# Kernel tuning notes

Hardware: AMD Instinct MI355X
Metric: run time of the kernel (lower is better)

## Reference

```python
import jax, jax.numpy as jnp
import numpy as np

B, L, DIM = 2, 1024, 512
HEADS = 8
D = DIM // HEADS
FORE_DIM, POST_DIM = 256, 1024
L_FORE, L_POST = 4 * L, L // 4


def setup_inputs() -> dict:
    key = jax.random.key(0)
    ks = jax.random.split(key, 8)
    s = 0.02  # weight init scale
    return {
        "x": jax.random.normal(ks[0], (B, L, DIM), jnp.float32),
        "fore_x": jax.random.normal(ks[1], (B, L_FORE, FORE_DIM), jnp.float32),
        "post_x": jax.random.normal(ks[2], (B, L_POST, POST_DIM), jnp.float32),
        # Linear weights stored [in, out] (transposed vs torch nn.Linear)
        "wq": jax.random.normal(ks[3], (DIM, DIM), jnp.float32) * s,
        "bq": jnp.zeros((DIM,), jnp.float32),
        "wkv1": jax.random.normal(ks[4], (FORE_DIM, 2 * DIM), jnp.float32) * s,
        "bkv1": jnp.zeros((2 * DIM,), jnp.float32),
        "wkv2": jax.random.normal(ks[5], (POST_DIM, 2 * DIM), jnp.float32) * s,
        "bkv2": jnp.zeros((2 * DIM,), jnp.float32),
        "wproj": jax.random.normal(ks[6], (3 * DIM, DIM), jnp.float32) * s,
        "bproj": jnp.zeros((DIM,), jnp.float32),
    }


def reference(x, fore_x, post_x, wq, bq, wkv1, bkv1, wkv2, bkv2, wproj, bproj):
    scale = D ** (-0.5)
    # q: [B, H, L, D], pre-scaled as in the torch code
    q = (x @ wq + bq).reshape(B, L, HEADS, D).transpose(0, 2, 1, 3) * scale

    def cross_attn(ctx, w, b):
        # ctx: [B, Lc, Cin] -> k, v: [B, H, Lc, D]
        kv = (ctx @ w + b).reshape(B, ctx.shape[1], 2, HEADS, D)
        k = kv[:, :, 0].transpose(0, 2, 1, 3)
        v = kv[:, :, 1].transpose(0, 2, 1, 3)
        attn = jax.nn.softmax(jnp.einsum("bhqd,bhkd->bhqk", q, k), axis=-1)
        out = jnp.einsum("bhqk,bhkd->bhqd", attn, v)
        return out.transpose(0, 2, 1, 3).reshape(B, L, DIM)

    x_2 = cross_attn(post_x, wkv2, bkv2)
    x_1 = cross_attn(fore_x, wkv1, bkv1)
    cat = jnp.concatenate([x, x_1, x_2], axis=2)  # [B, L, 3*DIM]
    return cat @ wproj + bproj
```

## Files before the change

kernel.cpp:

```cpp
#include <hip/hip_runtime.h>
#include <hip/hip_bf16.h>
#include <stdint.h>

typedef __attribute__((ext_vector_type(8))) short bf8;
typedef __attribute__((ext_vector_type(4))) short bf4;
typedef __attribute__((ext_vector_type(2))) short bf2;
typedef __attribute__((ext_vector_type(4))) float f32x4;

__device__ inline short f2bf(float f) {
  union { __hip_bfloat16 h; short s; } u;
  u.h = __float2bfloat16(f);
  return u.s;
}
__device__ inline float bf2f(short s) {
  union { short s; __hip_bfloat16 h; } u;
  u.s = s;
  return __bfloat162float(u.h);
}

__device__ inline f32x4 mfma16(bf8 a, bf8 b, f32x4 c) {
  return __builtin_amdgcn_mfma_f32_16x16x32_bf16(a, b, c, 0, 0, 0);
}

__global__ __launch_bounds__(256) void mega1_k(
    const float* __restrict__ x, const float* __restrict__ fore,
    const float* __restrict__ post,
    const float* __restrict__ wq, const float* __restrict__ wkv1,
    const float* __restrict__ bkv1, const float* __restrict__ wkv2,
    const float* __restrict__ wproj,
    short* __restrict__ kv1, short* __restrict__ cat,
    float* __restrict__ qpart, float* __restrict__ kv2part,
    short* __restrict__ wT)
{
  __shared__ __align__(16) short a_lds[2][128 * 40];
  __shared__ __align__(16) short b_lds[2][64 * 40];
  const int bid = blockIdx.x, tid = threadIdx.x;

  if (bid >= 1536) {
    float (*tl)[65] = reinterpret_cast<float(*)[65]>(&a_lds[0][0]);
    int tb = bid - 1536;
    int kt = tb % 24, nt = tb / 24;
    int k0 = kt * 64, n0 = nt * 64;
    int kr = tid >> 2, c4 = tid & 3;
#pragma unroll
    for (int i = 0; i < 4; ++i) {
      int cc = c4 + i * 4;
      float4 v = *(const float4*)&wproj[(size_t)(k0 + kr) * 512 + n0 + cc * 4];
      tl[kr][cc * 4 + 0] = v.x; tl[kr][cc * 4 + 1] = v.y;
      tl[kr][cc * 4 + 2] = v.z; tl[kr][cc * 4 + 3] = v.w;
    }
    __syncthreads();
    int nr = tid >> 2, p = tid & 3;
#pragma unroll
    for (int i = 0; i < 2; ++i) {
      int kk = p * 16 + i * 8;
      bf8 o;
#pragma unroll
      for (int j = 0; j < 8; ++j) o[j] = f2bf(tl[kk + j][nr]);
      *(bf8*)&wT[(size_t)(n0 + nr) * 1536 + k0 + kk] = o;
    }
    return;
  }

  const float *A, *W, *bias = nullptr;
  short* out = nullptr;
  float* outf = nullptr;
  int N, lda, ldo, m0, n0, koff;
  bool wcat = false, bf16out;
  if (bid < 1024) {
    A = fore; W = wkv1; bias = bkv1; out = kv1;
    N = 1024; lda = 256; ldo = 1024; koff = 0;
    m0 = (bid >> 4) * 128; n0 = (bid & 15) * 64; bf16out = true;
  } else if (bid < 1280) {
    int j = bid - 1024; int kc = j >> 7; j &= 127;
    A = x; W = wq; outf = qpart + (size_t)kc * (2048 * 512);
    N = 512; lda = 512; ldo = 512; koff = kc * 256;
    m0 = (j >> 3) * 128; n0 = (j & 7) * 64; bf16out = false;
    wcat = (j & 7) == 0;
  } else {
    int j = bid - 1280; int kc = j >> 6; j &= 63;
    A = post; W = wkv2; outf = kv2part + (size_t)kc * (512 * 1024);
    N = 1024; lda = 1024; ldo = 1024; koff = kc * 256;
    m0 = (j >> 4) * 128; n0 = (j & 15) * 64; bf16out = false;
  }

  const int w = tid >> 6, lane = tid & 63, g = lane >> 4, lr = lane & 15;
  const int wrow = w & 1, wcol = w >> 1;

  f32x4 z = {0.f, 0.f, 0.f, 0.f};
  f32x4 acc[4][2];
#pragma unroll
  for (int mi = 0; mi < 4; ++mi)
#pragma unroll
    for (int ni = 0; ni < 2; ++ni) acc[mi][ni] = z;

  const int arow = tid >> 3, ac4 = tid & 7;
  const int bcol = tid & 63, bj4 = tid >> 6;

  float4 ra[4], rna[4];
  float rw[8], rnw[8];

  auto LOADA = [&](int kg, float4* af, float* wg) {
#pragma unroll
    for (int i = 0; i < 4; ++i)
      af[i] = *(const float4*)&A[(size_t)(m0 + arow + 32 * i) * lda + kg + ac4 * 4];
#pragma unroll
    for (int j = 0; j < 8; ++j)
      wg[j] = W[(size_t)(kg + bj4 * 8 + j) * N + n0 + bcol];
  };
  auto STAGE = [&](int b, const float4* af, const float* wg, int kg) {
#pragma unroll
    for (int i = 0; i < 4; ++i) {
      int rr = arow + 32 * i;
      int s = (ac4 >> 1) ^ (rr & 3);
      bf4 o;
      o[0] = f2bf(af[i].x); o[1] = f2bf(af[i].y);
      o[2] = f2bf(af[i].z); o[3] = f2bf(af[i].w);
      *(bf4*)&a_lds[b][rr * 40 + s * 8 + (ac4 & 1) * 4] = o;
      if (wcat)
        *(bf4*)&cat[(size_t)(m0 + rr) * 1536 + kg + ac4 * 4] = o;
    }
    int s = bj4 ^ (bcol & 3);
    bf8 o;
#pragma unroll
    for (int j = 0; j < 8; ++j) o[j] = f2bf(wg[j]);
    *(bf8*)&b_lds[b][bcol * 40 + s * 8] = o;
  };

  LOADA(koff, ra, rw);
  STAGE(0, ra, rw, koff);
  LOADA(koff + 32, rna, rnw);
  __syncthreads();

#pragma unroll
  for (int it = 0; it < 8; ++it) {
    if (it < 7) STAGE((it + 1) & 1, rna, rnw, koff + (it + 1) * 32);
    if (it < 6) LOADA(koff + (it + 2) * 32, rna, rnw);

    const int b = it & 1;
    bf8 afr[4], bfr[2];
#pragma unroll
    for (int mi = 0; mi < 4; ++mi) {
      int row = wrow * 64 + mi * 16 + lr;
      afr[mi] = *(const bf8*)&a_lds[b][row * 40 + ((g ^ (row & 3)) << 3)];
    }
#pragma unroll
    for (int ni = 0; ni < 2; ++ni) {
      int col = wcol * 32 + ni * 16 + lr;
      bfr[ni] = *(const bf8*)&b_lds[b][col * 40 + ((g ^ (col & 3)) << 3)];
    }
#pragma unroll
    for (int mi = 0; mi < 4; ++mi)
#pragma unroll
      for (int ni = 0; ni < 2; ++ni)
        acc[mi][ni] = mfma16(afr[mi], bfr[ni], acc[mi][ni]);
    __syncthreads();
  }

#pragma unroll
  for (int ni = 0; ni < 2; ++ni) {
    int col = n0 + wcol * 32 + ni * 16 + lr;
    float bv = bf16out ? bias[col] : 0.f;
#pragma unroll
    for (int mi = 0; mi < 4; ++mi) {
      int rowb = m0 + wrow * 64 + mi * 16 + g * 4;
#pragma unroll
      for (int r = 0; r < 4; ++r) {
        float val = acc[mi][ni][r] + bv;
        if (bf16out)
          out[(size_t)(rowb + r) * ldo + col] = f2bf(val);
        else
          outf[(size_t)(rowb + r) * ldo + col] = val;
      }
    }
  }
}

__global__ __launch_bounds__(256) void finalize_k(
    const float* __restrict__ qpart, const float* __restrict__ kv2part,
    const float* __restrict__ bq, const float* __restrict__ bkv2,
    short* __restrict__ qb, short* __restrict__ kv2)
{
  const int bid = blockIdx.x, tid = threadIdx.x;
  if (bid < 1024) {
    int i = bid * 256 + tid;
    const float qsc = 0.125f * 1.44269504088896f;
    float4 a = ((const float4*)qpart)[i];
    float4 b = ((const float4*)qpart)[i + 262144];
    int col = (i * 4) & 511;
    float4 bv = *(const float4*)&bq[col];
    bf4 o;
    o[0] = f2bf((a.x + b.x + bv.x) * qsc);
    o[1] = f2bf((a.y + b.y + bv.y) * qsc);
    o[2] = f2bf((a.z + b.z + bv.z) * qsc);
    o[3] = f2bf((a.w + b.w + bv.w) * qsc);
    ((bf4*)qb)[i] = o;
  } else {
    int j = (bid - 1024) * 256 + tid;
    float4 a = ((const float4*)kv2part)[j];
    float4 b = ((const float4*)kv2part)[j + 131072];
    float4 c = ((const float4*)kv2part)[j + 262144];
    float4 d = ((const float4*)kv2part)[j + 393216];
    int col = (j * 4) & 1023;
    float4 bv = *(const float4*)&bkv2[col];
    bf4 o;
    o[0] = f2bf(a.x + b.x + c.x + d.x + bv.x);
    o[1] = f2bf(a.y + b.y + c.y + d.y + bv.y);
    o[2] = f2bf(a.z + b.z + c.z + d.z + bv.z);
    o[3] = f2bf(a.w + b.w + c.w + d.w + bv.w);
    ((bf4*)kv2)[j] = o;
  }
}

__global__ __launch_bounds__(256) void attn_k(
    const short* __restrict__ q,
    const short* __restrict__ kv1, const short* __restrict__ kv2,
    short* __restrict__ o1, float* __restrict__ l1,
    short* __restrict__ cat)
{
  __shared__ __align__(16) short k_lds[64 * 64];
  __shared__ __align__(16) short v_lds[64 * 72];
  const int tid = threadIdx.x;
  const int w = tid >> 6, lane = tid & 63, g = lane >> 4, lr = lane & 15;

  const int bid = blockIdx.x;
  const short* kvsrc;
  int qt, h, bb, split, chunk, Lc;
  bool direct;
  if (bid < 512) {
    qt = bid >> 6; int j = bid & 63;
    h = j & 7; int zz = j >> 3;
    bb = zz >> 2; split = zz & 3;
    kvsrc = kv1; chunk = 1024; Lc = 4096; direct = false;
  } else {
    int j2 = bid - 512;
    qt = j2 >> 4; int r = j2 & 15;
    h = r & 7; bb = r >> 3; split = 0;
    kvsrc = kv2; chunk = 256; Lc = 256; direct = true;
  }

  const int qbase = bb * 1024 + qt * 128 + w * 32;
  bf8 qfA[2], qfB[2];
#pragma unroll
  for (int s2 = 0; s2 < 2; ++s2) {
    const short* qp = &q[(size_t)(qbase + s2 * 16 + lr) * 512 + h * 64];
    qfA[s2] = *(const bf8*)&qp[g * 8];
    qfB[s2] = *(const bf8*)&qp[32 + g * 8];
  }

  const f32x4 z = {0.f, 0.f, 0.f, 0.f};
  f32x4 oaccT[2][4];
#pragma unroll
  for (int s2 = 0; s2 < 2; ++s2)
#pragma unroll
    for (int i = 0; i < 4; ++i) oaccT[s2][i] = z;
  float lsum_l[2] = {0.f, 0.f};

  const short* kvb = kvsrc + (size_t)bb * Lc * 1024 + (size_t)split * chunk * 1024;

  const int krow = tid >> 2, ksl = tid & 3;
  const short* kgp = kvb + (size_t)krow * 1024 + h * 64;
  const int vi = tid & 31, vj = tid >> 5;
  const short* vgp = kvb + (size_t)(2 * vi) * 1024 + 512 + h * 64 + vj * 8;
  const int lc0 = 2 * vi;
  const int vpos = (lc0 & 32) + ((lc0 & 12) << 1) + ((lc0 & 16) >> 2) + (lc0 & 3);

  bf8 k0c, k1c, v0c, v1c;
  k0c = *(const bf8*)(kgp + ksl * 8);
  k1c = *(const bf8*)(kgp + (ksl + 4) * 8);
  v0c = *(const bf8*)vgp;
  v1c = *(const bf8*)(vgp + 1024);

  const int nit = chunk >> 6;
  for (int it = 0; it < nit; ++it) {
    __syncthreads();
    *(bf8*)&k_lds[krow * 64 + ((ksl ^ (krow & 7)) << 3)] = k0c;
    *(bf8*)&k_lds[krow * 64 + (((ksl + 4) ^ (krow & 7)) << 3)] = k1c;
#pragma unroll
    for (int jj = 0; jj < 8; ++jj) {
      int d = vj * 8 + jj;
      bf2 pr; pr[0] = v0c[jj]; pr[1] = v1c[jj];
      *(bf2*)&v_lds[d * 72 + vpos] = pr;
    }
    __syncthreads();
    if (it + 1 < nit) {
      size_t off = (size_t)64 * 1024 * (it + 1);
      k0c = *(const bf8*)(kgp + off + ksl * 8);
      k1c = *(const bf8*)(kgp + off + (ksl + 4) * 8);
      v0c = *(const bf8*)(vgp + off);
      v1c = *(const bf8*)(vgp + off + 1024);
    }

    f32x4 sv[2][4];
#pragma unroll
    for (int t = 0; t < 4; ++t) {
      int lc = t * 16 + lr;
      bf8 kf0 = *(const bf8*)&k_lds[lc * 64 + ((g ^ (lc & 7)) << 3)];
      bf8 kf1 = *(const bf8*)&k_lds[lc * 64 + (((4 + g) ^ (lc & 7)) << 3)];
#pragma unroll
      for (int s2 = 0; s2 < 2; ++s2) {
        sv[s2][t] = mfma16(kf0, qfA[s2], z);
        sv[s2][t] = mfma16(kf1, qfB[s2], sv[s2][t]);
      }
    }

    bf8 pb[2][2];
#pragma unroll
    for (int s2 = 0; s2 < 2; ++s2) {
      float acc_l = 0.f;
#pragma unroll
      for (int t = 0; t < 4; ++t) {
        float p0 = exp2f(sv[s2][t][0]);
        float p1 = exp2f(sv[s2][t][1]);
        float p2 = exp2f(sv[s2][t][2]);
        float p3 = exp2f(sv[s2][t][3]);
        acc_l += (p0 + p1) + (p2 + p3);
        int c = t >> 1, hb = (t & 1) * 4;
        pb[s2][c][hb + 0] = f2bf(p0);
        pb[s2][c][hb + 1] = f2bf(p1);
        pb[s2][c][hb + 2] = f2bf(p2);
        pb[s2][c][hb + 3] = f2bf(p3);
      }
      lsum_l[s2] += acc_l;
    }

#pragma unroll
    for (int dt = 0; dt < 4; ++dt) {
      int d = dt * 16 + lr;
      bf8 vf0 = *(const bf8*)&v_lds[d * 72 + 8 * g];
      bf8 vf1 = *(const bf8*)&v_lds[d * 72 + 32 + 8 * g];
      oaccT[0][dt] = mfma16(vf0, pb[0][0], oaccT[0][dt]);
      oaccT[0][dt] = mfma16(vf1, pb[0][1], oaccT[0][dt]);
      oaccT[1][dt] = mfma16(vf0, pb[1][0], oaccT[1][dt]);
      oaccT[1][dt] = mfma16(vf1, pb[1][1], oaccT[1][dt]);
    }
  }

  if (direct) {
#pragma unroll
    for (int s2 = 0; s2 < 2; ++s2) {
      float t = lsum_l[s2];
      t += __shfl_xor(t, 16);
      t += __shfl_xor(t, 32);
      float rle = 1.f / t;
      int qrow = qbase + s2 * 16 + lr;
#pragma unroll
      for (int dt = 0; dt < 4; ++dt) {
        bf4 o4;
#pragma unroll
        for (int r = 0; r < 4; ++r) o4[r] = f2bf(oaccT[s2][dt][r] * rle);
        *(bf4*)&cat[(size_t)qrow * 1536 + 1024 + h * 64 + dt * 16 + 4 * g] = o4;
      }
    }
    return;
  }

#pragma unroll
  for (int s2 = 0; s2 < 2; ++s2) {
    int prow = (bb * 8 + h) * 1024 + qt * 128 + w * 32 + s2 * 16 + lr;
    short* ob = o1 + ((size_t)split * 16384 + prow) * 64;
#pragma unroll
    for (int dt = 0; dt < 4; ++dt) {
      bf4 o4;
#pragma unroll
      for (int r = 0; r < 4; ++r) o4[r] = f2bf(oaccT[s2][dt][r]);
      *(bf4*)&ob[dt * 16 + 4 * g] = o4;
    }
    float t = lsum_l[s2];
    t += __shfl_xor(t, 16);
    t += __shfl_xor(t, 32);
    if (g == 0) l1[(size_t)split * 16384 + prow] = t;
  }
}

__global__ __launch_bounds__(256) void comb_k(
    const short* __restrict__ o1, const float* __restrict__ l1,
    short* __restrict__ cat)
{
  int row = blockIdx.x * 32 + (threadIdx.x >> 3);
  int d8 = (threadIdx.x & 7) * 8;
  float l = 0.f;
#pragma unroll
  for (int s = 0; s < 4; ++s) l += l1[(size_t)s * 16384 + row];
  float acc[8] = {};
#pragma unroll
  for (int s = 0; s < 4; ++s) {
    bf8 v = *(const bf8*)&o1[((size_t)s * 16384 + row) * 64 + d8];
#pragma unroll
    for (int j = 0; j < 8; ++j) acc[j] += bf2f(v[j]);
  }
  float rle = 1.f / l;
  bf8 o;
#pragma unroll
  for (int j = 0; j < 8; ++j) o[j] = f2bf(acc[j] * rle);
  int bb = row >> 13, h = (row >> 10) & 7, qr = row & 1023;
  *(bf8*)&cat[(size_t)(bb * 1024 + qr) * 1536 + 512 + h * 64 + d8] = o;
}

__global__ __launch_bounds__(256) void gemmo_k(
    const short* __restrict__ A, const short* __restrict__ wT,
    const float* __restrict__ bias, float* __restrict__ out)
{
  __shared__ __align__(16) short a_lds[2][64 * 40];
  __shared__ __align__(16) short b_lds[2][64 * 40];
  const int tid = threadIdx.x;
  const int w = tid >> 6, lane = tid & 63, g = lane >> 4, lr = lane & 15;
  const int id = blockIdx.x;
  const int m = ((id >> 3) & 3) | ((id & 7) << 2);
  const int n = id >> 5;
  const int m0 = m * 64, n0 = n * 64;
  const int K = 1536;

  f32x4 z = {0.f, 0.f, 0.f, 0.f};
  f32x4 acc[4];
#pragma unroll
  for (int mi = 0; mi < 4; ++mi) acc[mi] = z;

  const int arow = tid >> 2, ac8 = tid & 3;
  const int bcol = tid & 63, bj4 = tid >> 6;
  bf8 ra, rna, rb, rnb;

  auto LOADAB = [&](int kg, bf8& ab, bf8& bb) {
    ab = *(const bf8*)&A[(size_t)(m0 + arow) * K + kg + ac8 * 8];
    bb = *(const bf8*)&wT[(size_t)(n0 + bcol) * K + kg + bj4 * 8];
  };
  auto STAGE = [&](int b, bf8 ab, bf8 bb) {
    *(bf8*)&a_lds[b][arow * 40 + ((ac8 ^ (arow & 3)) << 3)] = ab;
    *(bf8*)&b_lds[b][bcol * 40 + ((bj4 ^ (bcol & 3)) << 3)] = bb;
  };

  const int nit = K >> 5;
  LOADAB(0, ra, rb);
  STAGE(0, ra, rb);
  LOADAB(32, rna, rnb);
  __syncthreads();

  for (int it = 0; it < nit; ++it) {
    if (it + 1 < nit) STAGE((it + 1) & 1, rna, rnb);
    if (it + 2 < nit) LOADAB((it + 2) * 32, rna, rnb);

    const int b = it & 1;
    bf8 afr[4], bfr;
#pragma unroll
    for (int mi = 0; mi < 4; ++mi) {
      int row = mi * 16 + lr;
      afr[mi] = *(const bf8*)&a_lds[b][row * 40 + ((g ^ (row & 3)) << 3)];
    }
    {
      int col = w * 16 + lr;
      bfr = *(const bf8*)&b_lds[b][col * 40 + ((g ^ (col & 3)) << 3)];
    }
#pragma unroll
    for (int mi = 0; mi < 4; ++mi) acc[mi] = mfma16(afr[mi], bfr, acc[mi]);
    __syncthreads();
  }

  {
    int col = n0 + w * 16 + lr;
    float bv = bias[col];
#pragma unroll
    for (int mi = 0; mi < 4; ++mi) {
      int rowb = m0 + mi * 16 + g * 4;
#pragma unroll
      for (int r = 0; r < 4; ++r)
        out[(size_t)(rowb + r) * 512 + col] = acc[mi][r] + bv;
    }
  }
}

extern "C" void kernel_launch(void* const* d_in, const int* in_sizes, int n_in,
                              void* d_out, int out_size, void* d_ws, size_t ws_size,
                              hipStream_t stream) {
  const float* x     = (const float*)d_in[0];
  const float* fore  = (const float*)d_in[1];
  const float* post  = (const float*)d_in[2];
  const float* wq    = (const float*)d_in[3];
  const float* bq    = (const float*)d_in[4];
  const float* wkv1  = (const float*)d_in[5];
  const float* bkv1  = (const float*)d_in[6];
  const float* wkv2  = (const float*)d_in[7];
  const float* bkv2  = (const float*)d_in[8];
  const float* wproj = (const float*)d_in[9];
  const float* bproj = (const float*)d_in[10];

  char* ws = (char*)d_ws;
  short* qb      = (short*)ws;
  short* kv1     = (short*)(ws + (2ull << 20));
  short* kv2     = (short*)(ws + (18ull << 20));
  short* cat     = (short*)(ws + (19ull << 20));
  short* o1      = (short*)(ws + (25ull << 20));
  float* l1      = (float*)(ws + (33ull << 20));
  float* qpart   = (float*)(ws + (34ull << 20));
  float* kv2part = (float*)(ws + (42ull << 20));
  short* wT      = (short*)(ws + (50ull << 20));

  mega1_k<<<1728, 256, 0, stream>>>(x, fore, post, wq, wkv1, bkv1, wkv2,
                                    wproj, kv1, cat, qpart, kv2part, wT);
  finalize_k<<<1536, 256, 0, stream>>>(qpart, kv2part, bq, bkv2, qb, kv2);
  attn_k<<<640, 256, 0, stream>>>(qb, kv1, kv2, o1, l1, cat);
  comb_k<<<512, 256, 0, stream>>>(o1, l1, cat);
  gemmo_k<<<256, 256, 0, stream>>>(cat, wT, bproj, (float*)d_out);
}
```

Before: 93.17 us.

## Drop split-K projection partials and finalize kernel; split fore attention eight ways

The Q and post-KV projections no longer split K into fp32 partial buffers that a separate finalize kernel summed. Each tile now loops over the full K and applies bias, scale and bf16 conversion in its own epilogue, so one launch and the fp32 partial round-trip go away. Long-K blocks are scheduled first so they are not left running alone at the end. The fore-context attention now splits across 8 key chunks instead of 4, doubling its block count, and the combine step sums 8 partials. The cost is fewer, longer projection blocks and more partial-output traffic for the combine.

Result: faster. 86.05 us (-7.6%).

```diff
diff --git a/kernel.cpp b/kernel.cpp
--- a/kernel.cpp
+++ b/kernel.cpp
@@ -25,20 +25,20 @@
 __global__ __launch_bounds__(256) void mega1_k(
     const float* __restrict__ x, const float* __restrict__ fore,
     const float* __restrict__ post,
-    const float* __restrict__ wq, const float* __restrict__ wkv1,
-    const float* __restrict__ bkv1, const float* __restrict__ wkv2,
+    const float* __restrict__ wq, const float* __restrict__ bq,
+    const float* __restrict__ wkv1, const float* __restrict__ bkv1,
+    const float* __restrict__ wkv2, const float* __restrict__ bkv2,
     const float* __restrict__ wproj,
-    short* __restrict__ kv1, short* __restrict__ cat,
-    float* __restrict__ qpart, float* __restrict__ kv2part,
-    short* __restrict__ wT)
+    short* __restrict__ qb, short* __restrict__ kv1, short* __restrict__ kv2,
+    short* __restrict__ cat, short* __restrict__ wT)
 {
   __shared__ __align__(16) short a_lds[2][128 * 40];
   __shared__ __align__(16) short b_lds[2][64 * 40];
   const int bid = blockIdx.x, tid = threadIdx.x;
 
-  if (bid >= 1536) {
+  if (bid >= 1216) {
     float (*tl)[65] = reinterpret_cast<float(*)[65]>(&a_lds[0][0]);
-    int tb = bid - 1536;
+    int tb = bid - 1216;
     int kt = tb % 24, nt = tb / 24;
     int k0 = kt * 64, n0 = nt * 64;
     int kr = tid >> 2, c4 = tid & 3;
@@ -62,26 +62,27 @@
     return;
   }
 
-  const float *A, *W, *bias = nullptr;
-  short* out = nullptr;
-  float* outf = nullptr;
-  int N, lda, ldo, m0, n0, koff;
-  bool wcat = false, bf16out;
-  if (bid < 1024) {
-    A = fore; W = wkv1; bias = bkv1; out = kv1;
-    N = 1024; lda = 256; ldo = 1024; koff = 0;
-    m0 = (bid >> 4) * 128; n0 = (bid & 15) * 64; bf16out = true;
-  } else if (bid < 1280) {
-    int j = bid - 1024; int kc = j >> 7; j &= 127;
-    A = x; W = wq; outf = qpart + (size_t)kc * (2048 * 512);
-    N = 512; lda = 512; ldo = 512; koff = kc * 256;
-    m0 = (j >> 3) * 128; n0 = (j & 7) * 64; bf16out = false;
+  const float *A, *W, *bias;
+  short* out;
+  int N, lda, ldo, m0, n0, K;
+  float osc = 1.f;
+  bool wcat = false;
+  if (bid < 64) {
+    A = post; W = wkv2; bias = bkv2; out = kv2;
+    N = 1024; lda = 1024; ldo = 1024; K = 1024;
+    m0 = (bid >> 4) * 128; n0 = (bid & 15) * 64;
+  } else if (bid < 192) {
+    int j = bid - 64;
+    A = x; W = wq; bias = bq; out = qb;
+    N = 512; lda = 512; ldo = 512; K = 512;
+    m0 = (j >> 3) * 128; n0 = (j & 7) * 64;
+    osc = 0.125f * 1.44269504088896f;
     wcat = (j & 7) == 0;
   } else {
-    int j = bid - 1280; int kc = j >> 6; j &= 63;
-    A = post; W = wkv2; outf = kv2part + (size_t)kc * (512 * 1024);
-    N = 1024; lda = 1024; ldo = 1024; koff = kc * 256;
-    m0 = (j >> 4) * 128; n0 = (j & 15) * 64; bf16out = false;
+    int j = bid - 192;
+    A = fore; W = wkv1; bias = bkv1; out = kv1;
+    N = 1024; lda = 256; ldo = 1024; K = 256;
+    m0 = (j >> 4) * 128; n0 = (j & 15) * 64;
   }
 
   const int w = tid >> 6, lane = tid & 63, g = lane >> 4, lr = lane & 15;
@@ -127,15 +128,15 @@
     *(bf8*)&b_lds[b][bcol * 40 + s * 8] = o;
   };
 
-  LOADA(koff, ra, rw);
-  STAGE(0, ra, rw, koff);
-  LOADA(koff + 32, rna, rnw);
+  const int nit = K >> 5;
+  LOADA(0, ra, rw);
+  STAGE(0, ra, rw, 0);
+  LOADA(32, rna, rnw);
   __syncthreads();
 
-#pragma unroll
-  for (int it = 0; it < 8; ++it) {
-    if (it < 7) STAGE((it + 1) & 1, rna, rnw, koff + (it + 1) * 32);
-    if (it < 6) LOADA(koff + (it + 2) * 32, rna, rnw);
+  for (int it = 0; it < nit; ++it) {
+    if (it + 1 < nit) STAGE((it + 1) & 1, rna, rnw, (it + 1) * 32);
+    if (it + 2 < nit) LOADA((it + 2) * 32, rna, rnw);
 
     const int b = it & 1;
     bf8 afr[4], bfr[2];
@@ -160,55 +161,14 @@
 #pragma unroll
   for (int ni = 0; ni < 2; ++ni) {
     int col = n0 + wcol * 32 + ni * 16 + lr;
-    float bv = bf16out ? bias[col] : 0.f;
+    float bv = bias[col];
 #pragma unroll
     for (int mi = 0; mi < 4; ++mi) {
       int rowb = m0 + wrow * 64 + mi * 16 + g * 4;
 #pragma unroll
-      for (int r = 0; r < 4; ++r) {
-        float val = acc[mi][ni][r] + bv;
-        if (bf16out)
-          out[(size_t)(rowb + r) * ldo + col] = f2bf(val);
-        else
-          outf[(size_t)(rowb + r) * ldo + col] = val;
-      }
-    }
-  }
-}
-
-__global__ __launch_bounds__(256) void finalize_k(
-    const float* __restrict__ qpart, const float* __restrict__ kv2part,
-    const float* __restrict__ bq, const float* __restrict__ bkv2,
-    short* __restrict__ qb, short* __restrict__ kv2)
-{
-  const int bid = blockIdx.x, tid = threadIdx.x;
-  if (bid < 1024) {
-    int i = bid * 256 + tid;
-    const float qsc = 0.125f * 1.44269504088896f;
-    float4 a = ((const float4*)qpart)[i];
-    float4 b = ((const float4*)qpart)[i + 262144];
-    int col = (i * 4) & 511;
-    float4 bv = *(const float4*)&bq[col];
-    bf4 o;
-    o[0] = f2bf((a.x + b.x + bv.x) * qsc);
-    o[1] = f2bf((a.y + b.y + bv.y) * qsc);
-    o[2] = f2bf((a.z + b.z + bv.z) * qsc);
-    o[3] = f2bf((a.w + b.w + bv.w) * qsc);
-    ((bf4*)qb)[i] = o;
-  } else {
-    int j = (bid - 1024) * 256 + tid;
-    float4 a = ((const float4*)kv2part)[j];
-    float4 b = ((const float4*)kv2part)[j + 131072];
-    float4 c = ((const float4*)kv2part)[j + 262144];
-    float4 d = ((const float4*)kv2part)[j + 393216];
-    int col = (j * 4) & 1023;
-    float4 bv = *(const float4*)&bkv2[col];
-    bf4 o;
-    o[0] = f2bf(a.x + b.x + c.x + d.x + bv.x);
-    o[1] = f2bf(a.y + b.y + c.y + d.y + bv.y);
-    o[2] = f2bf(a.z + b.z + c.z + d.z + bv.z);
-    o[3] = f2bf(a.w + b.w + c.w + d.w + bv.w);
-    ((bf4*)kv2)[j] = o;
+      for (int r = 0; r < 4; ++r)
+        out[(size_t)(rowb + r) * ldo + col] = f2bf((acc[mi][ni][r] + bv) * osc);
+    }
   }
 }
 
@@ -227,13 +187,13 @@
   const short* kvsrc;
   int qt, h, bb, split, chunk, Lc;
   bool direct;
-  if (bid < 512) {
-    qt = bid >> 6; int j = bid & 63;
+  if (bid < 1024) {
+    qt = bid >> 7; int j = bid & 127;
     h = j & 7; int zz = j >> 3;
-    bb = zz >> 2; split = zz & 3;
-    kvsrc = kv1; chunk = 1024; Lc = 4096; direct = false;
+    bb = zz >> 3; split = zz & 7;
+    kvsrc = kv1; chunk = 512; Lc = 4096; direct = false;
   } else {
-    int j2 = bid - 512;
+    int j2 = bid - 1024;
     qt = j2 >> 4; int r = j2 & 15;
     h = r & 7; bb = r >> 3; split = 0;
     kvsrc = kv2; chunk = 256; Lc = 256; direct = true;
@@ -381,10 +341,10 @@
   int d8 = (threadIdx.x & 7) * 8;
   float l = 0.f;
 #pragma unroll
-  for (int s = 0; s < 4; ++s) l += l1[(size_t)s * 16384 + row];
+  for (int s = 0; s < 8; ++s) l += l1[(size_t)s * 16384 + row];
   float acc[8] = {};
 #pragma unroll
-  for (int s = 0; s < 4; ++s) {
+  for (int s = 0; s < 8; ++s) {
     bf8 v = *(const bf8*)&o1[((size_t)s * 16384 + row) * 64 + d8];
 #pragma unroll
     for (int j = 0; j < 8; ++j) acc[j] += bf2f(v[j]);
@@ -484,20 +444,17 @@
   const float* bproj = (const float*)d_in[10];
 
   char* ws = (char*)d_ws;
-  short* qb      = (short*)ws;
-  short* kv1     = (short*)(ws + (2ull << 20));
-  short* kv2     = (short*)(ws + (18ull << 20));
-  short* cat     = (short*)(ws + (19ull << 20));
-  short* o1      = (short*)(ws + (25ull << 20));
-  float* l1      = (float*)(ws + (33ull << 20));
-  float* qpart   = (float*)(ws + (34ull << 20));
-  float* kv2part = (float*)(ws + (42ull << 20));
-  short* wT      = (short*)(ws + (50ull << 20));
-
-  mega1_k<<<1728, 256, 0, stream>>>(x, fore, post, wq, wkv1, bkv1, wkv2,
-                                    wproj, kv1, cat, qpart, kv2part, wT);
-  finalize_k<<<1536, 256, 0, stream>>>(qpart, kv2part, bq, bkv2, qb, kv2);
-  attn_k<<<640, 256, 0, stream>>>(qb, kv1, kv2, o1, l1, cat);
+  short* qb  = (short*)ws;
+  short* kv1 = (short*)(ws + (2ull << 20));
+  short* kv2 = (short*)(ws + (18ull << 20));
+  short* cat = (short*)(ws + (19ull << 20));
+  short* o1  = (short*)(ws + (25ull << 20));
+  float* l1  = (float*)(ws + (41ull << 20));
+  short* wT  = (short*)(ws + (42ull << 20));
+
+  mega1_k<<<1408, 256, 0, stream>>>(x, fore, post, wq, bq, wkv1, bkv1,
+                                    wkv2, bkv2, wproj, qb, kv1, kv2, cat, wT);
+  attn_k<<<1152, 256, 0, stream>>>(qb, kv1, kv2, o1, l1, cat);
   comb_k<<<512, 256, 0, stream>>>(o1, l1, cat);
   gemmo_k<<<256, 256, 0, stream>>>(cat, wT, bproj, (float*)d_out);
 }
```
